# Optimization experiments

Measured on AMD Instinct MI355X. Metric: run time of the kernel, lower is better.

The kernel has to match this reference:

```python
import jax, jax.numpy as jnp
import numpy as np

NPOINT = 1024   # number of sampled centers
NSAMPLE = 32    # neighbors per center
BN_EPS = 1e-5


def setup_inputs() -> dict:
    key = jax.random.key(0)
    ks = jax.random.split(key, 6)
    B, N, C = 8, 4096, 6
    inp = {
        "xyz": jax.random.normal(ks[0], (B, N, 3), jnp.float32),
        "points": jax.random.normal(ks[1], (B, N, C), jnp.float32),
        "W0": jax.random.normal(ks[2], (64, 9), jnp.float32) * 0.1,
        "g0": jnp.ones((64,), jnp.float32),
        "b0": jnp.zeros((64,), jnp.float32),
        "W1": jax.random.normal(ks[3], (64, 64), jnp.float32) * 0.1,
        "g1": jnp.ones((64,), jnp.float32),
        "b1": jnp.zeros((64,), jnp.float32),
        "W2": jax.random.normal(ks[4], (128, 64), jnp.float32) * 0.1,
        "g2": jnp.ones((128,), jnp.float32),
        "b2": jnp.zeros((128,), jnp.float32),
    }
    return inp


def sample_and_group(xyz, points):
    # xyz: [B,N,3], points: [B,N,C]
    B, N, _ = xyz.shape
    stride = N // NPOINT
    new_xyz = xyz[:, ::stride]                      # [B,S,3] deterministic subsample (FPS surrogate)
    # squared pairwise distances via ||a||^2 + ||b||^2 - 2 a.b  -> [B,S,N]
    d = (jnp.sum(new_xyz * new_xyz, -1)[:, :, None]
         + jnp.sum(xyz * xyz, -1)[:, None, :]
         - 2.0 * jnp.einsum('bsd,bnd->bsn', new_xyz, xyz))
    _, idx = jax.lax.top_k(-d, NSAMPLE)             # [B,S,K] KNN indices
    gather = jax.vmap(lambda arr, i: arr[i])        # per-batch gather: [N,C],[S,K] -> [S,K,C]
    g_xyz = gather(xyz, idx) - new_xyz[:, :, None, :]   # relative coords [B,S,K,3]
    g_pts = gather(points, idx)                     # [B,S,K,C]
    new_points = jnp.concatenate([g_xyz, g_pts], -1)    # [B,S,K,3+C]
    return new_xyz, new_points


def mlp_layer(x, W, g, b):
    # Conv2d(1x1, bias=False) == channel contraction; BN2d with batch stats; ReLU
    x = jnp.einsum('bskc,oc->bsko', x, W)
    m = jnp.mean(x, axis=(0, 1, 2))
    v = jnp.var(x, axis=(0, 1, 2))
    x = (x - m) * jax.lax.rsqrt(v + BN_EPS) * g + b
    return jax.nn.relu(x)


def reference(xyz, points, W0, g0, b0, W1, g1, b1, W2, g2, b2):
    new_xyz, x = sample_and_group(xyz, points)      # x: [B,S,K,9]
    x = mlp_layer(x, W0, g0, b0)
    x = mlp_layer(x, W1, g1, b1)
    x = mlp_layer(x, W2, g2, b2)
    new_points = jnp.max(x, axis=2)                 # max-pool over neighbor dim K -> [B,S,128]
    return new_xyz, new_points
```

## Files before the change

### kernel.cpp

```cpp
#include <hip/hip_runtime.h>
#include <float.h>
#include <stdint.h>

#define TOT   262144
#define NPTS  4096
#define KNN   32
#define BN_EPS 1e-5f
#define CAPV  64

typedef _Float16 f16;
typedef _Float16 f16x2 __attribute__((ext_vector_type(2)));
typedef _Float16 f16x4 __attribute__((ext_vector_type(4)));
typedef _Float16 f16x8 __attribute__((ext_vector_type(8)));
typedef float    f32x4 __attribute__((ext_vector_type(4)));

__device__ __forceinline__ int mbcnt64(unsigned long long m){
  return __builtin_amdgcn_mbcnt_hi((unsigned)(m>>32),
         __builtin_amdgcn_mbcnt_lo((unsigned)(m & 0xffffffffull), 0));
}
__device__ __forceinline__ unsigned f2ord(float f){
  unsigned u = __float_as_uint(f);
  return u ^ (((unsigned)((int)u >> 31)) | 0x80000000u);
}
__device__ __forceinline__ f16x2 bnrelu2(f16x2 x, f16x2 a, f16x2 c){
  f16x2 r = x*a + c;
  const f16 z = (f16)0.f;
  r[0] = r[0] > z ? r[0] : z;
  r[1] = r[1] > z ? r[1] : z;
  return r;
}
__device__ __forceinline__ void writeElem(int n, int e, float qx, float qy, float qz,
    const float4* __restrict__ xb, const float* __restrict__ fb,
    f16* __restrict__ grouped, f16* __restrict__ g16){
  float4 P = xb[n];
  f16 a[16];
  a[0]=(f16)(P.x-qx); a[1]=(f16)(P.y-qy); a[2]=(f16)(P.z-qz);
  #pragma unroll
  for (int c6=0;c6<6;c6++) a[3+c6] = (f16)fb[n*6+c6];
  #pragma unroll
  for (int i=9;i<16;i++) a[i]=(f16)0.f;
  #pragma unroll
  for (int c=0;c<9;c++) grouped[c*TOT+e] = a[c];
  f16x8 lo, hi;
  #pragma unroll
  for (int i=0;i<8;i++){ lo[i]=a[i]; hi[i]=a[8+i]; }
  *(f16x8*)(g16 + (size_t)e*16)     = lo;
  *(f16x8*)(g16 + (size_t)e*16 + 8) = hi;
}

__global__ __launch_bounds__(256) void prep(const float* __restrict__ xyz,
    float4* __restrict__ xyzp){
  int p = blockIdx.x*256 + threadIdx.x;
  float x = xyz[p*3+0], y = xyz[p*3+1], z = xyz[p*3+2];
  xyzp[p] = make_float4(x, y, z, x*x+y*y+z*z);
}

__global__ __launch_bounds__(256) void knn_gather(
    const float4* __restrict__ xyzp, const float* __restrict__ pts,
    f16* __restrict__ grouped, f16* __restrict__ g16,
    float* __restrict__ out_newxyz){
  __shared__ unsigned wkbuf[4][4][CAPV];
  __shared__ unsigned short wibuf[4][4][CAPV];
  __shared__ unsigned lcnt[4][4];
  const int lane = threadIdx.x & 63;
  const int wv   = threadIdx.x >> 6;
  const int q0 = (blockIdx.x*4 + wv)*4;
  const int b = q0 >> 10, s0 = q0 & 1023;
  const float4* xb = xyzp + b*NPTS;
  float qx[4], qy[4], qz[4], qq[4];
  #pragma unroll
  for (int t=0;t<4;t++){
    float4 Q = xb[(s0+t)*4];
    qx[t]=Q.x; qy[t]=Q.y; qz[t]=Q.z; qq[t]=Q.w;
  }
  if (lane < 4) lcnt[wv][lane] = 0;
  if (lane == 0){
    #pragma unroll
    for (int t=0;t<4;t++){
      out_newxyz[(q0+t)*3+0]=qx[t]; out_newxyz[(q0+t)*3+1]=qy[t];
      out_newxyz[(q0+t)*3+2]=qz[t];
    }
  }

  unsigned mm[4] = {0xFFFFFFFFu,0xFFFFFFFFu,0xFFFFFFFFu,0xFFFFFFFFu};
  #pragma unroll 4
  for (int j=0;j<64;j++){
    float4 P = xb[j*64+lane];
    #pragma unroll
    for (int t=0;t<4;t++){
      float d = (qq[t]+P.w) - 2.f*(qx[t]*P.x+qy[t]*P.y+qz[t]*P.z);
      unsigned k = f2ord(d);
      mm[t] = k<mm[t] ? k : mm[t];
    }
  }
  unsigned sm[4] = {mm[0],mm[1],mm[2],mm[3]};
  #pragma unroll
  for (int k=2;k<=64;k<<=1){
    #pragma unroll
    for (int j=k>>1;j>0;j>>=1){
      bool keepmin = (((lane&k)==0) == ((lane&j)==0));
      #pragma unroll
      for (int t=0;t<4;t++){
        unsigned o = __shfl_xor(sm[t], j, 64);
        sm[t] = keepmin ? (sm[t]<o?sm[t]:o) : (sm[t]>o?sm[t]:o);
      }
    }
  }
  unsigned U[4];
  #pragma unroll
  for (int t=0;t<4;t++) U[t] = __shfl(sm[t], 31, 64);

  #pragma unroll 2
  for (int j=0;j<64;j++){
    float4 P = xb[j*64+lane];
    #pragma unroll
    for (int t=0;t<4;t++){
      float d = (qq[t]+P.w) - 2.f*(qx[t]*P.x+qy[t]*P.y+qz[t]*P.z);
      unsigned k = f2ord(d);
      if (k <= U[t]){
        unsigned p = atomicAdd(&lcnt[wv][t], 1u);
        if (p < CAPV){ wkbuf[wv][t][p]=k; wibuf[wv][t][p]=(unsigned short)(j*64+lane); }
      }
    }
  }
  int cnt[4];
  #pragma unroll
  for (int t=0;t<4;t++) cnt[t] = (int)lcnt[wv][t];

  unsigned long long v[4];
  #pragma unroll
  for (int t=0;t<4;t++){
    unsigned myk = (lane<cnt[t]) ? wkbuf[wv][t][lane] : 0xFFFFFFFFu;
    unsigned myi = (lane<cnt[t]) ? wibuf[wv][t][lane] : 0u;
    v[t] = (((unsigned long long)myk)<<16) | myi;
  }
  #pragma unroll
  for (int k=2;k<=64;k<<=1){
    #pragma unroll
    for (int j=k>>1;j>0;j>>=1){
      bool keepmin = (((lane&k)==0) == ((lane&j)==0));
      #pragma unroll
      for (int t=0;t<4;t++){
        unsigned long long o = __shfl_xor(v[t], j, 64);
        v[t] = keepmin ? (v[t]<o?v[t]:o) : (v[t]>o?v[t]:o);
      }
    }
  }

  const float* fb = pts + (size_t)b*NPTS*6;
  #pragma unroll
  for (int t=0;t<4;t++){
    const int ebase = (q0+t)*KNN;
    if (cnt[t] <= CAPV){
      if (lane < KNN){
        int n = (int)(v[t] & 0xffffull);
        writeElem(n, ebase+lane, qx[t],qy[t],qz[t], xb, fb, grouped, g16);
      }
    } else {
      unsigned V=0;
      for (int bit=31; bit>=0; --bit){
        unsigned X = V | (1u<<bit);
        int c=0;
        for (int j=0;j<64;j++){
          float4 P = xb[j*64+lane];
          float d = (qq[t]+P.w) - 2.f*(qx[t]*P.x+qy[t]*P.y+qz[t]*P.z);
          c += __popcll(__ballot(f2ord(d) < X));
        }
        if (c < KNN) V = X;
      }
      int cnt2=0;
      for (int pass=0; pass<2; ++pass){
        for (int j=0;j<64;j++){
          float4 P = xb[j*64+lane];
          float d = (qq[t]+P.w) - 2.f*(qx[t]*P.x+qy[t]*P.y+qz[t]*P.z);
          unsigned kk = f2ord(d);
          bool sel = pass ? (kk==V) : (kk<V);
          unsigned long long msk = __ballot(sel);
          int pos = cnt2 + mbcnt64(msk);
          if (sel && pos < KNN)
            writeElem(j*64+lane, ebase+pos, qx[t],qy[t],qz[t], xb, fb, grouped, g16);
          cnt2 += __popcll(msk);
        }
      }
    }
  }
}

__global__ __launch_bounds__(256) void stats0m(const f16* __restrict__ grouped,
    float* __restrict__ s0m){
  const int lane = threadIdx.x & 63, wv = threadIdx.x >> 6;
  const int c = lane & 15, q = lane >> 4;
  const int base = (blockIdx.x*4 + wv)*512;
  f16x8 cfill = {};
  if (c == 9){
    #pragma unroll
    for (int i=0;i<8;i++) cfill[i] = (f16)1.f;
  }
  f32x4 acc = {0.f,0.f,0.f,0.f};
  #pragma unroll 4
  for (int chunk=0; chunk<16; ++chunk){
    int e = base + chunk*32 + q*8;
    f16x8 f = cfill;
    if (c < 9) f = *(const f16x8*)(grouped + (size_t)c*TOT + e);
    acc = __builtin_amdgcn_mfma_f32_16x16x32_f16(f, f, acc, 0,0,0);
  }
  __shared__ float red[4][16][16];
  #pragma unroll
  for (int i=0;i<4;i++) red[wv][q*4+i][c] = acc[i];
  __syncthreads();
  const int tid = threadIdx.x;
  if (tid < 160){
    int row = tid>>4, col = tid&15;
    float vv = red[0][row][col]+red[1][row][col]+red[2][row][col]+red[3][row][col];
    atomicAdd(&s0m[tid], vv);
  }
}

__global__ void finalize0(const float* __restrict__ s0m,
    const float* __restrict__ W0, const float* __restrict__ g0,
    const float* __restrict__ b0, float* __restrict__ ac0,
    const float* __restrict__ W1, const float* __restrict__ W2,
    f16* __restrict__ W0h, f16* __restrict__ W1h, f16* __restrict__ W2h){
  const int tid = threadIdx.x;
  __shared__ float S[160];
  __shared__ float A0s[64];
  if (tid < 160) S[tid] = s0m[tid];
  __syncthreads();
  if (tid < 64){
    float w[9];
    #pragma unroll
    for (int c=0;c<9;c++) w[c]=W0[tid*9+c];
    const float inv = 1.f/(float)TOT;
    float m=0.f;
    #pragma unroll
    for (int c=0;c<9;c++) m = fmaf(w[c], S[c*16+9], m);
    m *= inv;
    float e2=0.f;
    #pragma unroll
    for (int c1=0;c1<9;c1++){
      float t=0.f;
      #pragma unroll
      for (int c2=0;c2<9;c2++) t = fmaf(w[c2], S[c1*16+c2], t);
      e2 = fmaf(w[c1], t, e2);
    }
    e2 *= inv;
    float var = e2 - m*m;
    float a = g0[tid]*rsqrtf(var + BN_EPS);
    ac0[tid]    = a;
    ac0[64+tid] = fmaf(-m, a, b0[tid]);
    A0s[tid]    = a;
  }
  __syncthreads();
  for (int i=tid; i<2048; i+=256){
    int o = i>>5, c = i&31;
    W0h[i] = (f16)(c<9 ? A0s[o]*W0[o*9+c] : 0.f);
  }
  for (int i=tid; i<4096; i+=256) W1h[i] = (f16)W1[i];
  for (int i=tid; i<8192; i+=256) W2h[i] = (f16)W2[i];
}

__global__ __launch_bounds__(256) void layer1s(
    const f16* __restrict__ g16, const f16* __restrict__ W0h,
    const f16* __restrict__ W1h, const float* __restrict__ ac0,
    float* __restrict__ s1g){
  __shared__ f16 hb0[4][16][80];
  __shared__ float sred[4][128];
  const int lane = threadIdx.x & 63, wv = threadIdx.x >> 6;
  const int e16 = lane & 15, q = lane >> 4;
  const int base = blockIdx.x*512 + wv*128;

  f16x8 A0[4];
  #pragma unroll
  for (int m=0;m<4;m++) A0[m] = *(const f16x8*)(W0h + (m*16+e16)*32 + q*8);
  f16x8 A1[4][2];
  #pragma unroll
  for (int m=0;m<4;m++)
    #pragma unroll
    for (int s=0;s<2;s++) A1[m][s] = *(const f16x8*)(W1h + (m*16+e16)*64 + s*32 + q*8);
  float c0i[4][4];
  #pragma unroll
  for (int m=0;m<4;m++)
    #pragma unroll
    for (int i=0;i<4;i++) c0i[m][i] = ac0[64 + m*16 + q*4 + i];
  float ssum[16], ssq[16];
  #pragma unroll
  for (int i=0;i<16;i++){ ssum[i]=0.f; ssq[i]=0.f; }

  #pragma unroll 1
  for (int sub=0; sub<8; ++sub){
    int elem = base + sub*16 + e16;
    f16x8 bg = {};
    if (q < 2) bg = *(const f16x8*)(g16 + (size_t)elem*16 + q*8);
    #pragma unroll
    for (int m=0;m<4;m++){
      f32x4 acc = {c0i[m][0], c0i[m][1], c0i[m][2], c0i[m][3]};
      acc = __builtin_amdgcn_mfma_f32_16x16x32_f16(A0[m], bg, acc, 0,0,0);
      f16x4 w;
      w[0]=(f16)fmaxf(acc[0],0.f); w[1]=(f16)fmaxf(acc[1],0.f);
      w[2]=(f16)fmaxf(acc[2],0.f); w[3]=(f16)fmaxf(acc[3],0.f);
      *(f16x4*)(&hb0[wv][e16][m*16 + q*4]) = w;
    }
    f32x4 acc2[4];
    #pragma unroll
    for (int m=0;m<4;m++) acc2[m] = (f32x4){0.f,0.f,0.f,0.f};
    #pragma unroll
    for (int s=0;s<2;s++){
      f16x8 bh = *(const f16x8*)(&hb0[wv][e16][s*32 + q*8]);
      #pragma unroll
      for (int m=0;m<4;m++)
        acc2[m] = __builtin_amdgcn_mfma_f32_16x16x32_f16(A1[m][s], bh, acc2[m], 0,0,0);
    }
    #pragma unroll
    for (int m=0;m<4;m++)
      #pragma unroll
      for (int i=0;i<4;i++){
        float x = acc2[m][i];
        ssum[m*4+i] += x;
        ssq[m*4+i]  = fmaf(x, x, ssq[m*4+i]);
      }
  }
  #pragma unroll
  for (int t=0;t<16;t++){
    float a = ssum[t], bq = ssq[t];
    #pragma unroll
    for (int off=1; off<16; off<<=1){
      a  += __shfl_xor(a,  off, 64);
      bq += __shfl_xor(bq, off, 64);
    }
    ssum[t]=a; ssq[t]=bq;
  }
  if (e16==0){
    #pragma unroll
    for (int m=0;m<4;m++)
      #pragma unroll
      for (int i=0;i<4;i++){
        int ch = m*16 + q*4 + i;
        sred[wv][ch]    = ssum[m*4+i];
        sred[wv][64+ch] = ssq[m*4+i];
      }
  }
  __syncthreads();
  const int tid = threadIdx.x;
  if (tid < 128){
    float v = sred[0][tid]+sred[1][tid]+sred[2][tid]+sred[3][tid];
    atomicAdd(&s1g[tid], v);
  }
}

__global__ __launch_bounds__(256) void layer2max(
    const f16* __restrict__ g16, const f16* __restrict__ W0h,
    const f16* __restrict__ W1h, const f16* __restrict__ W2h,
    const float* __restrict__ ac0, const float* __restrict__ s1g,
    const float* __restrict__ g1, const float* __restrict__ b1,
    float* __restrict__ maxbuf, float* __restrict__ s2g){
  __shared__ f16 hb0[4][16][80];
  __shared__ f16 hb1[4][16][80];
  __shared__ f16 ac1s[128];
  __shared__ float lds[4][256];
  const int tid = threadIdx.x;
  const int lane = tid & 63, wv = tid >> 6;
  const int e16 = lane & 15, q = lane >> 4;
  if (tid < 64){
    const float inv = 1.f/(float)TOT;
    float m = s1g[tid]*inv;
    float vv = s1g[64+tid]*inv - m*m;
    float a = g1[tid]*rsqrtf(vv + BN_EPS);
    ac1s[tid]    = (f16)a;
    ac1s[64+tid] = (f16)fmaf(-m, a, b1[tid]);
  }
  __syncthreads();

  f16x8 A0[4];
  #pragma unroll
  for (int m=0;m<4;m++) A0[m] = *(const f16x8*)(W0h + (m*16+e16)*32 + q*8);
  f16x8 A1[4][2];
  #pragma unroll
  for (int m=0;m<4;m++)
    #pragma unroll
    for (int s=0;s<2;s++) A1[m][s] = *(const f16x8*)(W1h + (m*16+e16)*64 + s*32 + q*8);
  f16x8 Bw[8][2];
  #pragma unroll
  for (int nt=0;nt<8;nt++)
    #pragma unroll
    for (int s=0;s<2;s++) Bw[nt][s] = *(const f16x8*)(W2h + (nt*16+e16)*64 + s*32 + q*8);
  float c0i[4][4];
  #pragma unroll
  for (int m=0;m<4;m++)
    #pragma unroll
    for (int i=0;i<4;i++) c0i[m][i] = ac0[64 + m*16 + q*4 + i];
  f16x2 a1p[8], c1p[8];
  #pragma unroll
  for (int m=0;m<4;m++)
    #pragma unroll
    for (int j2=0;j2<2;j2++){
      a1p[m*2+j2] = ((const f16x2*)ac1s)[m*8 + q*2 + j2];
      c1p[m*2+j2] = ((const f16x2*)(ac1s+64))[m*8 + q*2 + j2];
    }
  float ssum[8], ssq[8];
  #pragma unroll
  for (int i=0;i<8;i++){ ssum[i]=0.f; ssq[i]=0.f; }

  #pragma unroll 1
  for (int qq=0; qq<4; ++qq){
    const int qid = blockIdx.x*16 + wv*4 + qq;
    f32x4 acc3[8][2];
    #pragma unroll
    for (int nt=0;nt<8;nt++){ acc3[nt][0]=(f32x4){0,0,0,0}; acc3[nt][1]=(f32x4){0,0,0,0}; }
    #pragma unroll 1
    for (int mt=0; mt<2; ++mt){
      int elem = qid*32 + mt*16 + e16;
      f16x8 bg = {};
      if (q < 2) bg = *(const f16x8*)(g16 + (size_t)elem*16 + q*8);
      #pragma unroll
      for (int m=0;m<4;m++){
        f32x4 acc = {c0i[m][0], c0i[m][1], c0i[m][2], c0i[m][3]};
        acc = __builtin_amdgcn_mfma_f32_16x16x32_f16(A0[m], bg, acc, 0,0,0);
        f16x4 w;
        w[0]=(f16)fmaxf(acc[0],0.f); w[1]=(f16)fmaxf(acc[1],0.f);
        w[2]=(f16)fmaxf(acc[2],0.f); w[3]=(f16)fmaxf(acc[3],0.f);
        *(f16x4*)(&hb0[wv][e16][m*16 + q*4]) = w;
      }
      f32x4 acc2[4];
      #pragma unroll
      for (int m=0;m<4;m++) acc2[m] = (f32x4){0.f,0.f,0.f,0.f};
      #pragma unroll
      for (int s=0;s<2;s++){
        f16x8 bh = *(const f16x8*)(&hb0[wv][e16][s*32 + q*8]);
        #pragma unroll
        for (int m=0;m<4;m++)
          acc2[m] = __builtin_amdgcn_mfma_f32_16x16x32_f16(A1[m][s], bh, acc2[m], 0,0,0);
      }
      #pragma unroll
      for (int m=0;m<4;m++){
        f16x2 p0 = bnrelu2((f16x2){(f16)acc2[m][0], (f16)acc2[m][1]}, a1p[m*2  ], c1p[m*2  ]);
        f16x2 p1 = bnrelu2((f16x2){(f16)acc2[m][2], (f16)acc2[m][3]}, a1p[m*2+1], c1p[m*2+1]);
        f16x4 w; w[0]=p0[0]; w[1]=p0[1]; w[2]=p1[0]; w[3]=p1[1];
        *(f16x4*)(&hb1[wv][e16][m*16 + q*4]) = w;
      }
      #pragma unroll
      for (int s=0;s<2;s++){
        f16x8 af = *(const f16x8*)(&hb1[wv][e16][s*32 + q*8]);
        #pragma unroll
        for (int nt=0;nt<8;nt++)
          acc3[nt][mt] = __builtin_amdgcn_mfma_f32_16x16x32_f16(af, Bw[nt][s], acc3[nt][mt], 0,0,0);
      }
    }
    float mx[8];
    #pragma unroll
    for (int nt=0;nt<8;nt++){
      f32x4 u = acc3[nt][0], vv = acc3[nt][1];
      float m1 = fmaxf(fmaxf(u[0],u[1]), fmaxf(u[2],u[3]));
      float m2 = fmaxf(fmaxf(vv[0],vv[1]), fmaxf(vv[2],vv[3]));
      mx[nt] = fmaxf(m1, m2);
      ssum[nt] += (u[0]+u[1])+(u[2]+u[3]) + (vv[0]+vv[1])+(vv[2]+vv[3]);
      float sq = 0.f;
      #pragma unroll
      for (int i=0;i<4;i++){ sq = fmaf(u[i],u[i],sq); sq = fmaf(vv[i],vv[i],sq); }
      ssq[nt] += sq;
      mx[nt] = fmaxf(mx[nt], __shfl_xor(mx[nt], 16, 64));
      mx[nt] = fmaxf(mx[nt], __shfl_xor(mx[nt], 32, 64));
    }
    if (lane < 16){
      #pragma unroll
      for (int nt=0;nt<8;nt++) maxbuf[(size_t)qid*128 + nt*16 + lane] = mx[nt];
    }
  }
  #pragma unroll
  for (int nt=0;nt<8;nt++){
    ssum[nt] += __shfl_xor(ssum[nt], 16, 64);
    ssum[nt] += __shfl_xor(ssum[nt], 32, 64);
    ssq[nt]  += __shfl_xor(ssq[nt], 16, 64);
    ssq[nt]  += __shfl_xor(ssq[nt], 32, 64);
  }
  if (q==0){
    #pragma unroll
    for (int nt=0;nt<8;nt++){
      lds[wv][nt*16+e16]     = ssum[nt];
      lds[wv][128+nt*16+e16] = ssq[nt];
    }
  }
  __syncthreads();
  float v = lds[0][tid]+lds[1][tid]+lds[2][tid]+lds[3][tid];
  atomicAdd(&s2g[tid], v);
}

__global__ __launch_bounds__(256) void apply2(
    const float* __restrict__ maxbuf, const float* __restrict__ s2g,
    const float* __restrict__ g2, const float* __restrict__ b2,
    float* __restrict__ outp){
  __shared__ float a2s[128], c2s[128];
  const int tid = threadIdx.x;
  if (tid < 128){
    const float inv = 1.f/(float)TOT;
    float m = s2g[tid]*inv;
    float v = s2g[128+tid]*inv - m*m;
    float a = g2[tid]*rsqrtf(v + BN_EPS);
    a2s[tid] = a;
    c2s[tid] = fmaf(-m, a, b2[tid]);
  }
  __syncthreads();
  int i = blockIdx.x*256 + tid;
  int o = i & 127;
  outp[i] = fmaxf(fmaf(maxbuf[i], a2s[o], c2s[o]), 0.f);
}

extern "C" void kernel_launch(void* const* d_in, const int* in_sizes, int n_in,
                              void* d_out, int out_size, void* d_ws, size_t ws_size,
                              hipStream_t stream){
  const float* xyz = (const float*)d_in[0];
  const float* pts = (const float*)d_in[1];
  const float* W0  = (const float*)d_in[2];
  const float* g0  = (const float*)d_in[3];
  const float* b0  = (const float*)d_in[4];
  const float* W1  = (const float*)d_in[5];
  const float* g1  = (const float*)d_in[6];
  const float* b1  = (const float*)d_in[7];
  const float* W2  = (const float*)d_in[8];
  const float* g2  = (const float*)d_in[9];
  const float* b2  = (const float*)d_in[10];
  float* out = (float*)d_out;

  float* ws      = (float*)d_ws;
  f16*   grouped = (f16*)ws;
  f16*   g16     = (f16*)(ws + (size_t)5*TOT);
  float* maxbuf  = ws + (size_t)13*TOT;
  float4* xyzp   = (float4*)(ws + (size_t)17*TOT);
  float* basep   = ws + (size_t)17*TOT + 131072;
  f16*   W0h     = (f16*)basep;
  f16*   W1h     = (f16*)(basep + 1024);
  f16*   W2h     = (f16*)(basep + 3072);
  float* s0m     = basep + 7168;
  float* s1g     = s0m + 160;
  float* s2g     = s1g + 128;
  float* ac0     = s2g + 256;

  (void)hipMemsetAsync(s0m, 0, 544*sizeof(float), stream);
  prep      <<< 128, 256, 0, stream>>>(xyz, xyzp);
  knn_gather<<< 512, 256, 0, stream>>>(xyzp, pts, grouped, g16, out);
  stats0m   <<< 128, 256, 0, stream>>>(grouped, s0m);
  finalize0 <<<   1, 256, 0, stream>>>(s0m, W0, g0, b0, ac0, W1, W2, W0h, W1h, W2h);
  layer1s   <<< 512, 256, 0, stream>>>(g16, W0h, W1h, ac0, s1g);
  layer2max <<< 512, 256, 0, stream>>>(g16, W0h, W1h, W2h, ac0, s1g, g1, b1, maxbuf, s2g);
  apply2    <<<4096, 256, 0, stream>>>(maxbuf, s2g, g2, b2, out + 24576);
}
```

Before: 243.1 us.

## Stage W0/W1 in LDS and split layer-3 accumulators to cut VGPR pressure

Both MLP kernels now copy the W0/W1 fragments and BN constants into shared memory once per block and reload them from LDS inside the loop, instead of holding them in registers for the whole kernel. In layer2max, the layer-2 outputs for both 16-row tiles are buffered in LDS first, and the 128-channel layer-3 MFMA is done in two groups of 64 channels, halving live accumulators. LDS row padding shrinks from 80 to 72. The aim is fewer VGPRs and higher occupancy, paid for with extra LDS traffic and a rolled loop inside the compute path.

```diff
diff --git a/kernel.cpp b/kernel.cpp
--- a/kernel.cpp
+++ b/kernel.cpp
@@ -263,25 +263,21 @@
     const f16* __restrict__ g16, const f16* __restrict__ W0h,
     const f16* __restrict__ W1h, const float* __restrict__ ac0,
     float* __restrict__ s1g){
-  __shared__ f16 hb0[4][16][80];
+  __shared__ f16 sW0[2048];
+  __shared__ f16 sW1[4096];
+  __shared__ float ac0c[64];
+  __shared__ f16 hb0[4][16][72];
   __shared__ float sred[4][128];
-  const int lane = threadIdx.x & 63, wv = threadIdx.x >> 6;
+  const int tid = threadIdx.x;
+  const int lane = tid & 63, wv = tid >> 6;
   const int e16 = lane & 15, q = lane >> 4;
+  *(f16x8*)(&sW0[tid*8]) = *(const f16x8*)(W0h + tid*8);
+  *(f16x8*)(&sW1[tid*8])        = *(const f16x8*)(W1h + tid*8);
+  *(f16x8*)(&sW1[2048 + tid*8]) = *(const f16x8*)(W1h + 2048 + tid*8);
+  if (tid < 64) ac0c[tid] = ac0[64+tid];
+  __syncthreads();
+
   const int base = blockIdx.x*512 + wv*128;
-
-  f16x8 A0[4];
-  #pragma unroll
-  for (int m=0;m<4;m++) A0[m] = *(const f16x8*)(W0h + (m*16+e16)*32 + q*8);
-  f16x8 A1[4][2];
-  #pragma unroll
-  for (int m=0;m<4;m++)
-    #pragma unroll
-    for (int s=0;s<2;s++) A1[m][s] = *(const f16x8*)(W1h + (m*16+e16)*64 + s*32 + q*8);
-  float c0i[4][4];
-  #pragma unroll
-  for (int m=0;m<4;m++)
-    #pragma unroll
-    for (int i=0;i<4;i++) c0i[m][i] = ac0[64 + m*16 + q*4 + i];
   float ssum[16], ssq[16];
   #pragma unroll
   for (int i=0;i<16;i++){ ssum[i]=0.f; ssq[i]=0.f; }
@@ -293,8 +289,9 @@
     if (q < 2) bg = *(const f16x8*)(g16 + (size_t)elem*16 + q*8);
     #pragma unroll
     for (int m=0;m<4;m++){
-      f32x4 acc = {c0i[m][0], c0i[m][1], c0i[m][2], c0i[m][3]};
-      acc = __builtin_amdgcn_mfma_f32_16x16x32_f16(A0[m], bg, acc, 0,0,0);
+      f32x4 acc = *(const f32x4*)(&ac0c[m*16 + q*4]);
+      f16x8 A0f = *(const f16x8*)(&sW0[(m*16+e16)*32 + q*8]);
+      acc = __builtin_amdgcn_mfma_f32_16x16x32_f16(A0f, bg, acc, 0,0,0);
       f16x4 w;
       w[0]=(f16)fmaxf(acc[0],0.f); w[1]=(f16)fmaxf(acc[1],0.f);
       w[2]=(f16)fmaxf(acc[2],0.f); w[3]=(f16)fmaxf(acc[3],0.f);
@@ -307,8 +304,10 @@
     for (int s=0;s<2;s++){
       f16x8 bh = *(const f16x8*)(&hb0[wv][e16][s*32 + q*8]);
       #pragma unroll
-      for (int m=0;m<4;m++)
-        acc2[m] = __builtin_amdgcn_mfma_f32_16x16x32_f16(A1[m][s], bh, acc2[m], 0,0,0);
+      for (int m=0;m<4;m++){
+        f16x8 A1f = *(const f16x8*)(&sW1[(m*16+e16)*64 + s*32 + q*8]);
+        acc2[m] = __builtin_amdgcn_mfma_f32_16x16x32_f16(A1f, bh, acc2[m], 0,0,0);
+      }
     }
     #pragma unroll
     for (int m=0;m<4;m++)
@@ -340,7 +339,6 @@
       }
   }
   __syncthreads();
-  const int tid = threadIdx.x;
   if (tid < 128){
     float v = sred[0][tid]+sred[1][tid]+sred[2][tid]+sred[3][tid];
     atomicAdd(&s1g[tid], v);
@@ -353,13 +351,20 @@
     const float* __restrict__ ac0, const float* __restrict__ s1g,
     const float* __restrict__ g1, const float* __restrict__ b1,
     float* __restrict__ maxbuf, float* __restrict__ s2g){
-  __shared__ f16 hb0[4][16][80];
-  __shared__ f16 hb1[4][16][80];
+  __shared__ f16 sW0[2048];
+  __shared__ f16 sW1[4096];
+  __shared__ float ac0c[64];
   __shared__ f16 ac1s[128];
+  __shared__ f16 hb0[4][16][72];
+  __shared__ f16 hb1[4][2][16][72];
   __shared__ float lds[4][256];
   const int tid = threadIdx.x;
   const int lane = tid & 63, wv = tid >> 6;
   const int e16 = lane & 15, q = lane >> 4;
+  *(f16x8*)(&sW0[tid*8]) = *(const f16x8*)(W0h + tid*8);
+  *(f16x8*)(&sW1[tid*8])        = *(const f16x8*)(W1h + tid*8);
+  *(f16x8*)(&sW1[2048 + tid*8]) = *(const f16x8*)(W1h + 2048 + tid*8);
+  if (tid < 64) ac0c[tid] = ac0[64+tid];
   if (tid < 64){
     const float inv = 1.f/(float)TOT;
     float m = s1g[tid]*inv;
@@ -370,32 +375,12 @@
   }
   __syncthreads();
 
-  f16x8 A0[4];
-  #pragma unroll
-  for (int m=0;m<4;m++) A0[m] = *(const f16x8*)(W0h + (m*16+e16)*32 + q*8);
-  f16x8 A1[4][2];
-  #pragma unroll
-  for (int m=0;m<4;m++)
-    #pragma unroll
-    for (int s=0;s<2;s++) A1[m][s] = *(const f16x8*)(W1h + (m*16+e16)*64 + s*32 + q*8);
   f16x8 Bw[8][2];
   #pragma unroll
   for (int nt=0;nt<8;nt++)
     #pragma unroll
     for (int s=0;s<2;s++) Bw[nt][s] = *(const f16x8*)(W2h + (nt*16+e16)*64 + s*32 + q*8);
-  float c0i[4][4];
-  #pragma unroll
-  for (int m=0;m<4;m++)
-    #pragma unroll
-    for (int i=0;i<4;i++) c0i[m][i] = ac0[64 + m*16 + q*4 + i];
-  f16x2 a1p[8], c1p[8];
-  #pragma unroll
-  for (int m=0;m<4;m++)
-    #pragma unroll
-    for (int j2=0;j2<2;j2++){
-      a1p[m*2+j2] = ((const f16x2*)ac1s)[m*8 + q*2 + j2];
-      c1p[m*2+j2] = ((const f16x2*)(ac1s+64))[m*8 + q*2 + j2];
-    }
+
   float ssum[8], ssq[8];
   #pragma unroll
   for (int i=0;i<8;i++){ ssum[i]=0.f; ssq[i]=0.f; }
@@ -403,9 +388,6 @@
   #pragma unroll 1
   for (int qq=0; qq<4; ++qq){
     const int qid = blockIdx.x*16 + wv*4 + qq;
-    f32x4 acc3[8][2];
-    #pragma unroll
-    for (int nt=0;nt<8;nt++){ acc3[nt][0]=(f32x4){0,0,0,0}; acc3[nt][1]=(f32x4){0,0,0,0}; }
     #pragma unroll 1
     for (int mt=0; mt<2; ++mt){
       int elem = qid*32 + mt*16 + e16;
@@ -413,8 +395,9 @@
       if (q < 2) bg = *(const f16x8*)(g16 + (size_t)elem*16 + q*8);
       #pragma unroll
       for (int m=0;m<4;m++){
-        f32x4 acc = {c0i[m][0], c0i[m][1], c0i[m][2], c0i[m][3]};
-        acc = __builtin_amdgcn_mfma_f32_16x16x32_f16(A0[m], bg, acc, 0,0,0);
+        f32x4 acc = *(const f32x4*)(&ac0c[m*16 + q*4]);
+        f16x8 A0f = *(const f16x8*)(&sW0[(m*16+e16)*32 + q*8]);
+        acc = __builtin_amdgcn_mfma_f32_16x16x32_f16(A0f, bg, acc, 0,0,0);
         f16x4 w;
         w[0]=(f16)fmaxf(acc[0],0.f); w[1]=(f16)fmaxf(acc[1],0.f);
         w[2]=(f16)fmaxf(acc[2],0.f); w[3]=(f16)fmaxf(acc[3],0.f);
@@ -427,38 +410,54 @@
       for (int s=0;s<2;s++){
         f16x8 bh = *(const f16x8*)(&hb0[wv][e16][s*32 + q*8]);
         #pragma unroll
-        for (int m=0;m<4;m++)
-          acc2[m] = __builtin_amdgcn_mfma_f32_16x16x32_f16(A1[m][s], bh, acc2[m], 0,0,0);
+        for (int m=0;m<4;m++){
+          f16x8 A1f = *(const f16x8*)(&sW1[(m*16+e16)*64 + s*32 + q*8]);
+          acc2[m] = __builtin_amdgcn_mfma_f32_16x16x32_f16(A1f, bh, acc2[m], 0,0,0);
+        }
       }
       #pragma unroll
       for (int m=0;m<4;m++){
-        f16x2 p0 = bnrelu2((f16x2){(f16)acc2[m][0], (f16)acc2[m][1]}, a1p[m*2  ], c1p[m*2  ]);
-        f16x2 p1 = bnrelu2((f16x2){(f16)acc2[m][2], (f16)acc2[m][3]}, a1p[m*2+1], c1p[m*2+1]);
+        f16x4 a4 = *(const f16x4*)(&ac1s[m*16 + q*4]);
+        f16x4 c4 = *(const f16x4*)(&ac1s[64 + m*16 + q*4]);
+        f16x2 p0 = bnrelu2((f16x2){(f16)acc2[m][0], (f16)acc2[m][1]},
+                           (f16x2){a4[0],a4[1]}, (f16x2){c4[0],c4[1]});
+        f16x2 p1 = bnrelu2((f16x2){(f16)acc2[m][2], (f16)acc2[m][3]},
+                           (f16x2){a4[2],a4[3]}, (f16x2){c4[2],c4[3]});
         f16x4 w; w[0]=p0[0]; w[1]=p0[1]; w[2]=p1[0]; w[3]=p1[1];
-        *(f16x4*)(&hb1[wv][e16][m*16 + q*4]) = w;
-      }
-      #pragma unroll
-      for (int s=0;s<2;s++){
-        f16x8 af = *(const f16x8*)(&hb1[wv][e16][s*32 + q*8]);
+        *(f16x4*)(&hb1[wv][mt][e16][m*16 + q*4]) = w;
+      }
+    }
+    float mx[8];
+    #pragma unroll 1
+    for (int g=0; g<2; ++g){
+      f32x4 acc3[4][2];
+      #pragma unroll
+      for (int j=0;j<4;j++){ acc3[j][0]=(f32x4){0,0,0,0}; acc3[j][1]=(f32x4){0,0,0,0}; }
+      #pragma unroll
+      for (int mt=0; mt<2; ++mt)
         #pragma unroll
-        for (int nt=0;nt<8;nt++)
-          acc3[nt][mt] = __builtin_amdgcn_mfma_f32_16x16x32_f16(af, Bw[nt][s], acc3[nt][mt], 0,0,0);
-      }
-    }
-    float mx[8];
-    #pragma unroll
-    for (int nt=0;nt<8;nt++){
-      f32x4 u = acc3[nt][0], vv = acc3[nt][1];
-      float m1 = fmaxf(fmaxf(u[0],u[1]), fmaxf(u[2],u[3]));
-      float m2 = fmaxf(fmaxf(vv[0],vv[1]), fmaxf(vv[2],vv[3]));
-      mx[nt] = fmaxf(m1, m2);
-      ssum[nt] += (u[0]+u[1])+(u[2]+u[3]) + (vv[0]+vv[1])+(vv[2]+vv[3]);
-      float sq = 0.f;
-      #pragma unroll
-      for (int i=0;i<4;i++){ sq = fmaf(u[i],u[i],sq); sq = fmaf(vv[i],vv[i],sq); }
-      ssq[nt] += sq;
-      mx[nt] = fmaxf(mx[nt], __shfl_xor(mx[nt], 16, 64));
-      mx[nt] = fmaxf(mx[nt], __shfl_xor(mx[nt], 32, 64));
+        for (int s=0;s<2;s++){
+          f16x8 af = *(const f16x8*)(&hb1[wv][mt][e16][s*32 + q*8]);
+          #pragma unroll
+          for (int j=0;j<4;j++)
+            acc3[j][mt] = __builtin_amdgcn_mfma_f32_16x16x32_f16(af, Bw[g*4+j][s], acc3[j][mt], 0,0,0);
+        }
+      #pragma unroll
+      for (int j=0;j<4;j++){
+        int nt = g*4 + j;
+        f32x4 u = acc3[j][0], vv = acc3[j][1];
+        float m1 = fmaxf(fmaxf(u[0],u[1]), fmaxf(u[2],u[3]));
+        float m2 = fmaxf(fmaxf(vv[0],vv[1]), fmaxf(vv[2],vv[3]));
+        float m = fmaxf(m1, m2);
+        ssum[nt] += (u[0]+u[1])+(u[2]+u[3]) + (vv[0]+vv[1])+(vv[2]+vv[3]);
+        float sq = 0.f;
+        #pragma unroll
+        for (int i=0;i<4;i++){ sq = fmaf(u[i],u[i],sq); sq = fmaf(vv[i],vv[i],sq); }
+        ssq[nt] += sq;
+        m = fmaxf(m, __shfl_xor(m, 16, 64));
+        m = fmaxf(m, __shfl_xor(m, 32, 64));
+        mx[nt] = m;
+      }
     }
     if (lane < 16){
       #pragma unroll
```

Measured after the change: 207.3 us. -14.7%, faster.
